# Kernel tuning notes

Measured on AMD Instinct MI355X. Metric: run time of the kernel, lower is better.

## Reference

```python
import jax, jax.numpy as jnp
import numpy as np
from jax import lax

INPUT_DIM = 12
T = 2048
H = 512
L = 6
EPS = 1e-5


def setup_inputs() -> dict:
    key = jax.random.key(0)
    ks = jax.random.split(key, 12)
    s = 1.0 / np.sqrt(H)
    inp = {
        "x": jax.random.normal(ks[0], (32, INPUT_DIM), dtype=jnp.float32),
        "in_proj_w": jax.random.normal(ks[1], (H, INPUT_DIM), dtype=jnp.float32) * (1.0 / np.sqrt(INPUT_DIM)),
        "in_proj_b": jnp.zeros((H,), dtype=jnp.float32),
        "W_ih": jax.random.uniform(ks[2], (L, 4 * H, H), dtype=jnp.float32, minval=-s, maxval=s),
        "W_hh": jax.random.uniform(ks[3], (L, 4 * H, H), dtype=jnp.float32, minval=-s, maxval=s),
        "b_ih": jax.random.uniform(ks[4], (L, 4 * H), dtype=jnp.float32, minval=-s, maxval=s),
        "b_hh": jax.random.uniform(ks[5], (L, 4 * H), dtype=jnp.float32, minval=-s, maxval=s),
        "ln_scale": jnp.ones((L, H), dtype=jnp.float32),
        "ln_bias": jnp.zeros((L, H), dtype=jnp.float32),
        "out_w": jax.random.normal(ks[6], (1, H), dtype=jnp.float32) * s,
        "out_b": jnp.zeros((1,), dtype=jnp.float32),
    }
    return inp


def _lstm_layer(h_in, Wih, Whh, bih, bhh):
    # h_in: (B, T, H); PyTorch gate order: i, f, g, o
    B = h_in.shape[0]
    xg = jnp.einsum("bth,gh->btg", h_in, Wih) + bih  # (B, T, 4H) input gates precomputed
    xg_t = jnp.swapaxes(xg, 0, 1)  # (T, B, 4H)
    h0 = jnp.zeros((B, H), dtype=h_in.dtype)
    c0 = jnp.zeros((B, H), dtype=h_in.dtype)

    def step(carry, xt):
        h, c = carry
        gates = xt + h @ Whh.T + bhh
        i, f, g, o = jnp.split(gates, 4, axis=-1)
        i = jax.nn.sigmoid(i)
        f = jax.nn.sigmoid(f)
        g = jnp.tanh(g)
        o = jax.nn.sigmoid(o)
        c = f * c + i * g
        h = o * jnp.tanh(c)
        return (h, c), h

    _, hs = lax.scan(step, (h0, c0), xg_t)  # hs: (T, B, H)
    return jnp.swapaxes(hs, 0, 1)


def _layernorm(x, scale, bias):
    mu = jnp.mean(x, axis=-1, keepdims=True)
    var = jnp.mean(jnp.square(x - mu), axis=-1, keepdims=True)
    return (x - mu) * lax.rsqrt(var + EPS) * scale + bias


def reference(x, in_proj_w, in_proj_b, W_ih, W_hh, b_ih, b_hh, ln_scale, ln_bias, out_w, out_b):
    x_proj = x @ in_proj_w.T + in_proj_b  # (B, H)
    h = jnp.broadcast_to(x_proj[:, None, :], (x.shape[0], T, H))  # repeat along time
    for l in range(L):
        out = _lstm_layer(h, W_ih[l], W_hh[l], b_ih[l], b_hh[l])
        h = _layernorm(out + h, ln_scale[l], ln_bias[l])  # dropout = identity (eval)
    y = jnp.einsum("bth,oh->bto", h, out_w) + out_b  # (B, T, 1)
    return y[..., 0]  # (B, T)
```

## Files before the change

kernel.cpp:

```cpp
#include <hip/hip_runtime.h>

typedef __attribute__((ext_vector_type(4))) int   i32x4;
typedef __attribute__((ext_vector_type(8))) short s16x8;
typedef __attribute__((ext_vector_type(4))) float f32x4;

__device__ __forceinline__ unsigned short f2bf(float f) {
  unsigned u = __float_as_uint(f);
  unsigned r = u + 0x7FFFu + ((u >> 16) & 1u);
  return (unsigned short)(r >> 16);
}
__device__ __forceinline__ unsigned pack2bf(float lo, float hi) {
  return (unsigned)f2bf(lo) | ((unsigned)f2bf(hi) << 16);
}
__device__ __forceinline__ float bflo(unsigned u){ return __uint_as_float(u << 16); }
__device__ __forceinline__ float bfhi(unsigned u){ return __uint_as_float(u & 0xFFFF0000u); }

__device__ __forceinline__ float sigm(float x){ return 1.0f / (1.0f + __expf(-x)); }
__device__ __forceinline__ float tanh_(float x){
  float ax = fabsf(x);
  float e  = __expf(-2.0f * ax);
  float t  = (1.0f - e) / (1.0f + e);
  return copysignf(t, x);
}

__device__ __forceinline__ unsigned long long aload(const unsigned long long* p) {
  return __hip_atomic_load(p, __ATOMIC_RELAXED, __HIP_MEMORY_SCOPE_AGENT);
}
__device__ __forceinline__ void astore32(unsigned* p, unsigned v) {
  __hip_atomic_store(p, v, __ATOMIC_RELAXED, __HIP_MEMORY_SCOPE_AGENT);
}
__device__ __forceinline__ void astore64(unsigned long long* p, unsigned long long v) {
  __hip_atomic_store(p, v, __ATOMIC_RELAXED, __HIP_MEMORY_SCOPE_AGENT);
}

__device__ __forceinline__ void waitflags(const unsigned* Flg, int base, unsigned need, int lane) {
  const unsigned* p = Flg + ((base + (lane & 31)) << 4);
  unsigned v = __hip_atomic_load(p, __ATOMIC_RELAXED, __HIP_MEMORY_SCOPE_AGENT);
  while (!__all((int)(v >= need))) {
    __builtin_amdgcn_s_sleep(1);
    v = __hip_atomic_load(p, __ATOMIC_RELAXED, __HIP_MEMORY_SCOPE_AGENT);
  }
}

__global__ __launch_bounds__(256) void k_inproj(const float* __restrict__ x,
                                                const float* __restrict__ w,
                                                const float* __restrict__ bb,
                                                float* __restrict__ XP) {
  int idx = blockIdx.x * 256 + threadIdx.x;
  int b = idx >> 9, j = idx & 511;
  float acc = bb[j];
#pragma unroll
  for (int k = 0; k < 12; ++k) acc += x[b * 12 + k] * w[j * 12 + k];
  XP[idx] = acc;
}

__global__ __launch_bounds__(256) void k_xg0(const float* __restrict__ XP,
                                             const float* __restrict__ Wih,
                                             const float* __restrict__ bih,
                                             float* __restrict__ XG0) {
  int idx = blockIdx.x * 256 + threadIdx.x;
  int b = idx & 31;
  int r = idx >> 5;
  const float* wr = Wih + (size_t)r * 512;
  const float* xr = XP + b * 512;
  float acc = bih[r];
  for (int k = 0; k < 512; k += 4) {
    const f32x4 w4 = *(const f32x4*)(wr + k);
    const f32x4 x4 = *(const f32x4*)(xr + k);
    acc += w4[0]*x4[0] + w4[1]*x4[1] + w4[2]*x4[2] + w4[3]*x4[3];
  }
  XG0[b * 2048 + r] = acc;
}

__global__ __launch_bounds__(256, 1) void k_pipe(
    const float* __restrict__ Wih, const float* __restrict__ Whh,
    const float* __restrict__ bih, const float* __restrict__ bhh,
    const float* __restrict__ lnS, const float* __restrict__ lnB,
    const float* __restrict__ XG0, const float* __restrict__ XP,
    unsigned long long* __restrict__ Hst,
    unsigned long long* __restrict__ Roll,
    unsigned long long* __restrict__ Part,
    unsigned* __restrict__ RB,
    unsigned* __restrict__ Flg,
    unsigned* __restrict__ Prog)
{
  __shared__ char smem[65536];
  const int tid   = threadIdx.x;
  const int wgid  = blockIdx.x;
  const int layer = wgid >> 5;
  const int w     = wgid & 31;

  char* xarea = smem;
  char* harea = smem + 32768;
  const int lane = tid & 63;
  const int wv   = tid >> 6;
  const int j0   = w << 4;
  float* gacc = (float*)(layer == 0 ? (smem + 10240) : (harea + 16384));

  unsigned long long* HstL = Hst + layer * 8192;

  s16x8 bfih[16], bfhh[16];
  {
    const int rcol = lane & 15;
    const int kg   = lane >> 4;
    const size_t rowbase = ((size_t)layer * 2048 + (size_t)(wv * 512 + j0 + rcol)) * 512;
    const float* ihr = Wih + rowbase;
    const float* hhr = Whh + rowbase;
#pragma unroll
    for (int kk = 0; kk < 16; ++kk) {
      const int k0 = kg * 8 + kk * 32;
      s16x8 v2;
#pragma unroll
      for (int j = 0; j < 8; ++j) v2[j] = (short)f2bf(hhr[k0 + j]);
      bfhh[kk] = v2;
      if (layer > 0) {
        s16x8 v1;
#pragma unroll
        for (int j = 0; j < 8; ++j) v1[j] = (short)f2bf(ihr[k0 + j]);
        bfih[kk] = v1;
      }
    }
  }

  const int ub = tid >> 3;
  const int jp = tid & 7;
  const int kpglob = (j0 >> 1) + jp;

  float bs[4][2];
#pragma unroll
  for (int g = 0; g < 4; ++g)
#pragma unroll
    for (int c = 0; c < 2; ++c) {
      const size_t r = (size_t)layer * 2048 + g * 512 + j0 + 2 * jp + c;
      float vv = bhh[r];
      if (layer > 0) vv += bih[r];
      bs[g][c] = vv;
    }

  float scp[4] = {0,0,0,0}, bip[4] = {0,0,0,0};
  if (layer > 0) {
    const int cb = (layer - 1) * 512 + 4 * (tid & 127);
#pragma unroll
    for (int j = 0; j < 4; ++j) { scp[j] = lnS[cb + j]; bip[j] = lnB[cb + j]; }
  }

  if (layer == 0) {
    float* xg0s = (float*)smem;
    float* xps  = (float*)(smem + 8192);
    for (int i = tid; i < 2048; i += 256) {
      int g = i >> 9, b = (i >> 4) & 31, jl = i & 15;
      xg0s[i] = XG0[b * 2048 + g * 512 + j0 + jl];
    }
    for (int i = tid; i < 512; i += 256) {
      int b = i >> 4, jl = i & 15;
      xps[i] = XP[b * 512 + j0 + jl];
    }
  }

  astore32((unsigned*)HstL + (ub << 8) + kpglob, 0u);
  __syncthreads();
  if (tid == 0)
    __hip_atomic_store(Flg + ((layer * 32 + w) << 4), 1u, __ATOMIC_RELEASE, __HIP_MEMORY_SCOPE_AGENT);

  float xinc0 = 0.f, xinc1 = 0.f;
  if (layer == 0) {
    const float* xps = (const float*)(smem + 8192);
    xinc0 = xps[ub * 16 + 2 * jp];
    xinc1 = xps[ub * 16 + 2 * jp + 1];
  }

  const int b31 = tid & 31, w8 = tid >> 5;

  if (layer > 0) {
    waitflags(Flg, (layer - 1) * 32, 2u, lane);
    const unsigned long long* RollC = Roll + (layer - 1) * 16384;
    const unsigned long long* PC    = Part + (layer - 1) * 4096;
    unsigned long long xr[16], pr[4];
#pragma unroll
    for (int it = 0; it < 16; ++it) xr[it] = aload(RollC + it * 256 + tid);
#pragma unroll
    for (int k = 0; k < 4; ++k) pr[k] = aload(PC + (w8 + 8 * k) * 32 + b31);
    float s4 = 0.f, ss4 = 0.f;
#pragma unroll
    for (int k = 0; k < 4; ++k) { s4 += __uint_as_float((unsigned)pr[k]); ss4 += __uint_as_float((unsigned)(pr[k] >> 32)); }
    float* scr = (float*)harea;
    scr[(w8 * 32 + b31) * 2]     = s4;
    scr[(w8 * 32 + b31) * 2 + 1] = ss4;
    __syncthreads();
    float* stats = (float*)(harea + 2048);
    if (tid < 32) {
      const float* sc = (const float*)harea;
      float ssum = 0.f, sssum = 0.f;
#pragma unroll
      for (int k = 0; k < 8; ++k) { ssum += sc[(k * 32 + tid) * 2]; sssum += sc[(k * 32 + tid) * 2 + 1]; }
      const float mu = ssum * (1.f / 512.f);
      float var = sssum * (1.f / 512.f) - mu * mu;
      stats[tid * 2] = mu; stats[tid * 2 + 1] = rsqrtf(var + 1e-5f);
    }
    __syncthreads();
#pragma unroll
    for (int it = 0; it < 16; ++it) {
      const int flat = it * 256 + tid;
      const int q = flat >> 7, c0 = (flat & 127) * 2;
      const float mu = stats[q * 2], rs = stats[q * 2 + 1];
      const unsigned lo = (unsigned)xr[it], hi = (unsigned)(xr[it] >> 32);
      const float a0 = (bflo(lo) - mu) * rs * scp[0] + bip[0];
      const float a1 = (bfhi(lo) - mu) * rs * scp[1] + bip[1];
      const float a2 = (bflo(hi) - mu) * rs * scp[2] + bip[2];
      const float a3 = (bfhi(hi) - mu) * rs * scp[3] + bip[3];
      *(unsigned long long*)(xarea + ((q * 1024 + c0 * 4) ^ ((q & 7) << 4))) =
          (unsigned long long)pack2bf(a0, a1) | ((unsigned long long)pack2bf(a2, a3) << 32);
    }
  }
  __syncthreads();

  const int rA  = lane & 15;
  const int kg2 = lane >> 4;
  const int swz = (rA & 7) << 4;
  const int ab0 = rA * 1024 + kg2 * 16;
  const int ab1 = ab0 + 16384;

  float creg0 = 0.f, creg1 = 0.f;
  unsigned myC = 0;
  const int lane31 = lane & 31;

#pragma unroll 1
  for (int t = 0; t < 2048; ++t) {
    if (layer < 5 && t >= 5) {
      const unsigned need = (unsigned)(t - 4);
      while (!__all((int)(myC >= need))) {
        if (myC < need)
          myC = __hip_atomic_load(Prog + (((layer + 1) * 32 + lane31) << 4),
                                  __ATOMIC_RELAXED, __HIP_MEMORY_SCOPE_AGENT);
        if (!__all((int)(myC >= need))) __builtin_amdgcn_s_sleep(1);
      }
    }

    waitflags(Flg, layer * 32, (unsigned)(t + 1), lane);

    const unsigned long long* hs = HstL + (size_t)(t & 1) * 4096;
    unsigned long long a[16];
#pragma unroll
    for (int it = 0; it < 16; ++it)
      a[it] = aload(hs + it * 256 + tid);

    float xin0, xin1;
    f32x4 ai0 = {0.f,0.f,0.f,0.f}, ai1 = {0.f,0.f,0.f,0.f};
    if (layer > 0) {
      const unsigned xu = *(const unsigned*)(xarea + (((ub * 1024) + kpglob * 4) ^ ((ub & 7) << 4)));
      xin0 = bflo(xu); xin1 = bfhi(xu);
#pragma unroll
      for (int kk = 0; kk < 16; ++kk) {
        const i32x4 x0 = *(const i32x4*)(xarea + ((ab0 + kk * 64) ^ swz));
        const i32x4 x1 = *(const i32x4*)(xarea + ((ab1 + kk * 64) ^ swz));
        ai0 = __builtin_amdgcn_mfma_f32_16x16x32_bf16(__builtin_bit_cast(s16x8, x0), bfih[kk], ai0, 0, 0, 0);
        ai1 = __builtin_amdgcn_mfma_f32_16x16x32_bf16(__builtin_bit_cast(s16x8, x1), bfih[kk], ai1, 0, 0, 0);
      }
    } else { xin0 = xinc0; xin1 = xinc1; }

#pragma unroll
    for (int it = 0; it < 16; ++it) {
      const int flat = it * 256 + tid;
      const int q = flat >> 7, kp2 = flat & 127;
      *(unsigned long long*)(harea + ((q * 1024 + kp2 * 8) ^ ((q & 7) << 4))) = a[it];
    }
    __syncthreads();

    f32x4 acc0, acc1;
    if (layer > 0) {
      f32x4 ah0 = {0.f,0.f,0.f,0.f}, ah1 = {0.f,0.f,0.f,0.f};
#pragma unroll
      for (int kk = 0; kk < 16; ++kk) {
        const i32x4 h0 = *(const i32x4*)(harea + ((ab0 + kk * 64) ^ swz));
        const i32x4 h1 = *(const i32x4*)(harea + ((ab1 + kk * 64) ^ swz));
        ah0 = __builtin_amdgcn_mfma_f32_16x16x32_bf16(__builtin_bit_cast(s16x8, h0), bfhh[kk], ah0, 0, 0, 0);
        ah1 = __builtin_amdgcn_mfma_f32_16x16x32_bf16(__builtin_bit_cast(s16x8, h1), bfhh[kk], ah1, 0, 0, 0);
      }
      acc0 = ai0 + ah0; acc1 = ai1 + ah1;
    } else {
      f32x4 a0a = {0.f,0.f,0.f,0.f}, a1a = {0.f,0.f,0.f,0.f};
      f32x4 a0b = {0.f,0.f,0.f,0.f}, a1b = {0.f,0.f,0.f,0.f};
#pragma unroll
      for (int kk = 0; kk < 8; ++kk) {
        const i32x4 h0a = *(const i32x4*)(harea + ((ab0 + kk * 64) ^ swz));
        const i32x4 h1a = *(const i32x4*)(harea + ((ab1 + kk * 64) ^ swz));
        const i32x4 h0b = *(const i32x4*)(harea + ((ab0 + (kk + 8) * 64) ^ swz));
        const i32x4 h1b = *(const i32x4*)(harea + ((ab1 + (kk + 8) * 64) ^ swz));
        a0a = __builtin_amdgcn_mfma_f32_16x16x32_bf16(__builtin_bit_cast(s16x8, h0a), bfhh[kk], a0a, 0, 0, 0);
        a1a = __builtin_amdgcn_mfma_f32_16x16x32_bf16(__builtin_bit_cast(s16x8, h1a), bfhh[kk], a1a, 0, 0, 0);
        a0b = __builtin_amdgcn_mfma_f32_16x16x32_bf16(__builtin_bit_cast(s16x8, h0b), bfhh[kk + 8], a0b, 0, 0, 0);
        a1b = __builtin_amdgcn_mfma_f32_16x16x32_bf16(__builtin_bit_cast(s16x8, h1b), bfhh[kk + 8], a1b, 0, 0, 0);
      }
      acc0 = a0a + a0b; acc1 = a1a + a1b;
    }
    __syncthreads();
    {
      float* gp = gacc + (wv * 16 + rA) * 36 + kg2 * 4;
      *(f32x4*)gp        = acc0;
      *(f32x4*)(gp + 16) = acc1;
    }
    __syncthreads();

    float pre[4][2];
#pragma unroll
    for (int g = 0; g < 4; ++g)
#pragma unroll
      for (int c = 0; c < 2; ++c) {
        float vv = gacc[(g * 16 + 2 * jp + c) * 36 + ub] + bs[g][c];
        if (layer == 0) vv += ((const float*)smem)[(g * 32 + ub) * 16 + 2 * jp + c];
        pre[g][c] = vv;
      }

    float i0 = sigm(pre[0][0]), ff0 = sigm(pre[1][0]), g0 = tanh_(pre[2][0]), o0 = sigm(pre[3][0]);
    creg0 = ff0 * creg0 + i0 * g0;
    float h0 = o0 * tanh_(creg0);
    float i1 = sigm(pre[0][1]), ff1 = sigm(pre[1][1]), g1 = tanh_(pre[2][1]), o1 = sigm(pre[3][1]);
    creg1 = ff1 * creg1 + i1 * g1;
    float h1 = o1 * tanh_(creg1);
    const float out0 = h0 + xin0, out1 = h1 + xin1;

    if (layer < 5) {
      float sP  = out0 + out1;
      float ssP = out0 * out0 + out1 * out1;
#pragma unroll
      for (int m = 1; m < 8; m <<= 1) { sP += __shfl_xor(sP, m, 64); ssP += __shfl_xor(ssP, m, 64); }
      astore32((unsigned*)(Roll + layer * 16384 + (size_t)(t & 3) * 4096) + (ub << 8) + kpglob,
               pack2bf(out0, out1));
      if (jp == 0)
        astore64(Part + layer * 4096 + (size_t)(t & 3) * 1024 + w * 32 + ub,
                 (unsigned long long)__float_as_uint(sP) |
                 ((unsigned long long)__float_as_uint(ssP) << 32));
    } else {
      RB[((size_t)ub * 2048 + t) * 256 + kpglob] = pack2bf(out0, out1);
    }
    astore32((unsigned*)(HstL + (size_t)((t + 1) & 1) * 4096) + (ub << 8) + kpglob,
             pack2bf(h0, h1));

    __syncthreads();
    if (tid == 0)
      __hip_atomic_store(Flg + ((layer * 32 + w) << 4), (unsigned)(t + 2),
                         __ATOMIC_RELEASE, __HIP_MEMORY_SCOPE_AGENT);

    if (layer > 0 && t < 2047) {
      waitflags(Flg, (layer - 1) * 32, (unsigned)(t + 3), lane);
      const unsigned long long* RollC = Roll + (layer - 1) * 16384 + (size_t)((t + 1) & 3) * 4096;
      const unsigned long long* PC    = Part + (layer - 1) * 4096 + (size_t)((t + 1) & 3) * 1024;
      unsigned long long xr[16], pr[4];
#pragma unroll
      for (int it = 0; it < 16; ++it) xr[it] = aload(RollC + it * 256 + tid);
#pragma unroll
      for (int k = 0; k < 4; ++k) pr[k] = aload(PC + (w8 + 8 * k) * 32 + b31);
      float s4 = 0.f, ss4 = 0.f;
#pragma unroll
      for (int k = 0; k < 4; ++k) { s4 += __uint_as_float((unsigned)pr[k]); ss4 += __uint_as_float((unsigned)(pr[k] >> 32)); }
      float* scr = (float*)harea;
      scr[(w8 * 32 + b31) * 2]     = s4;
      scr[(w8 * 32 + b31) * 2 + 1] = ss4;
      __syncthreads();
      float* stats = (float*)(harea + 2048);
      if (tid < 32) {
        const float* sc = (const float*)harea;
        float ssum = 0.f, sssum = 0.f;
#pragma unroll
        for (int k = 0; k < 8; ++k) { ssum += sc[(k * 32 + tid) * 2]; sssum += sc[(k * 32 + tid) * 2 + 1]; }
        const float mu = ssum * (1.f / 512.f);
        float var = sssum * (1.f / 512.f) - mu * mu;
        stats[tid * 2] = mu; stats[tid * 2 + 1] = rsqrtf(var + 1e-5f);
      }
      __syncthreads();
#pragma unroll
      for (int it = 0; it < 16; ++it) {
        const int flat = it * 256 + tid;
        const int q = flat >> 7, c0 = (flat & 127) * 2;
        const float mu = stats[q * 2], rs = stats[q * 2 + 1];
        const unsigned lo = (unsigned)xr[it], hi = (unsigned)(xr[it] >> 32);
        const float a0 = (bflo(lo) - mu) * rs * scp[0] + bip[0];
        const float a1 = (bfhi(lo) - mu) * rs * scp[1] + bip[1];
        const float a2 = (bflo(hi) - mu) * rs * scp[2] + bip[2];
        const float a3 = (bfhi(hi) - mu) * rs * scp[3] + bip[3];
        *(unsigned long long*)(xarea + ((q * 1024 + c0 * 4) ^ ((q & 7) << 4))) =
            (unsigned long long)pack2bf(a0, a1) | ((unsigned long long)pack2bf(a2, a3) << 32);
      }
      if (tid == 0)
        astore32(Prog + ((layer * 32 + w) << 4), (unsigned)(t + 1));
    }

    __syncthreads();
  }
}

__global__ __launch_bounds__(256) void k_lnout(const unsigned* __restrict__ Rin,
                                               const float* __restrict__ lnS,
                                               const float* __restrict__ lnB,
                                               const float* __restrict__ ow,
                                               const float* __restrict__ ob,
                                               float* __restrict__ y) {
  int row  = blockIdx.x * 4 + (threadIdx.x >> 6);
  int lane = threadIdx.x & 63;
  const i32x4 v = *(const i32x4*)(Rin + (size_t)row * 256 + lane * 4);
  float xv[8];
#pragma unroll
  for (int j = 0; j < 4; ++j) {
    unsigned u = (unsigned)v[j];
    xv[2*j]   = bflo(u);
    xv[2*j+1] = bfhi(u);
  }
  float s = 0.f, s2 = 0.f;
#pragma unroll
  for (int j = 0; j < 8; ++j) { s += xv[j]; s2 += xv[j] * xv[j]; }
#pragma unroll
  for (int m = 1; m < 64; m <<= 1) { s += __shfl_xor(s, m, 64); s2 += __shfl_xor(s2, m, 64); }
  float mu  = s * (1.f / 512.f);
  float var = s2 * (1.f / 512.f) - mu * mu;
  float rs  = rsqrtf(var + 1e-5f);
  const float* Sp = lnS + 5 * 512 + lane * 8;
  const float* Bp = lnB + 5 * 512 + lane * 8;
  const float* wp = ow + lane * 8;
  float acc = 0.f;
#pragma unroll
  for (int j = 0; j < 8; ++j)
    acc += ((xv[j] - mu) * rs * Sp[j] + Bp[j]) * wp[j];
#pragma unroll
  for (int m = 1; m < 64; m <<= 1) acc += __shfl_xor(acc, m, 64);
  if (lane == 0) y[row] = acc + ob[0];
}

extern "C" void kernel_launch(void* const* d_in, const int* in_sizes, int n_in,
                              void* d_out, int out_size, void* d_ws, size_t ws_size,
                              hipStream_t stream) {
  (void)in_sizes; (void)n_in; (void)out_size; (void)ws_size;
  const float* x   = (const float*)d_in[0];
  const float* ipw = (const float*)d_in[1];
  const float* ipb = (const float*)d_in[2];
  const float* Wih = (const float*)d_in[3];
  const float* Whh = (const float*)d_in[4];
  const float* bih = (const float*)d_in[5];
  const float* bhh = (const float*)d_in[6];
  const float* lnS = (const float*)d_in[7];
  const float* lnB = (const float*)d_in[8];
  const float* ow  = (const float*)d_in[9];
  const float* ob  = (const float*)d_in[10];
  float* y = (float*)d_out;

  char* ws = (char*)d_ws;
  unsigned* Flg             = (unsigned*)ws;
  unsigned* Prog            = (unsigned*)(ws + 16384);
  float* XP                 = (float*)(ws + 32768);
  float* XG0                = (float*)(ws + 98304);
  unsigned long long* Hst   = (unsigned long long*)(ws + 360448);
  unsigned long long* Roll  = (unsigned long long*)(ws + 753664);
  unsigned long long* Part  = (unsigned long long*)(ws + 1409024);
  unsigned* RB              = (unsigned*)(ws + 2097152);

  hipMemsetAsync(ws, 0, 32768, stream);
  k_inproj<<<64, 256, 0, stream>>>(x, ipw, ipb, XP);
  k_xg0<<<256, 256, 0, stream>>>(XP, Wih, bih, XG0);
  k_pipe<<<192, 256, 0, stream>>>(Wih, Whh, bih, bhh, lnS, lnB, XG0, XP,
                                  Hst, Roll, Part, RB, Flg, Prog);
  k_lnout<<<16384, 256, 0, stream>>>(RB, lnS, lnB, ow, ob, y);
}
```

Before: 18.25 ms.

## Compute layernorm stats locally per consumer, drop partial-sum exchange and barriers

Producers no longer publish per-block partial sums and sums of squares for the inter-layer layernorm. Each consumer loads a full 512-wide row per group of 8 lanes and reduces the statistics itself with wave shuffles, which removes the Part buffer, two __syncthreads and an LDS scratch reduction from every timestep. The wait and load of the next timestep's input is also moved ahead of the barrier and flag release, so it overlaps with the end of the current step. In exchange, the layernorm scale and bias are now read from global memory every step, and variance is computed from bf16-rounded values.

```diff
diff --git a/kernel.cpp b/kernel.cpp
--- a/kernel.cpp
+++ b/kernel.cpp
@@ -29,12 +29,9 @@
 __device__ __forceinline__ void astore32(unsigned* p, unsigned v) {
   __hip_atomic_store(p, v, __ATOMIC_RELAXED, __HIP_MEMORY_SCOPE_AGENT);
 }
-__device__ __forceinline__ void astore64(unsigned long long* p, unsigned long long v) {
-  __hip_atomic_store(p, v, __ATOMIC_RELAXED, __HIP_MEMORY_SCOPE_AGENT);
-}
-
-__device__ __forceinline__ void waitflags(const unsigned* Flg, int base, unsigned need, int lane) {
-  const unsigned* p = Flg + ((base + (lane & 31)) << 4);
+
+__device__ __forceinline__ void waitflags(const unsigned* F, int base, unsigned need, int lane) {
+  const unsigned* p = F + ((base + (lane & 31)) << 4);
   unsigned v = __hip_atomic_load(p, __ATOMIC_RELAXED, __HIP_MEMORY_SCOPE_AGENT);
   while (!__all((int)(v >= need))) {
     __builtin_amdgcn_s_sleep(1);
@@ -79,7 +76,6 @@
     const float* __restrict__ XG0, const float* __restrict__ XP,
     unsigned long long* __restrict__ Hst,
     unsigned long long* __restrict__ Roll,
-    unsigned long long* __restrict__ Part,
     unsigned* __restrict__ RB,
     unsigned* __restrict__ Flg,
     unsigned* __restrict__ Prog)
@@ -137,12 +133,8 @@
       bs[g][c] = vv;
     }
 
-  float scp[4] = {0,0,0,0}, bip[4] = {0,0,0,0};
-  if (layer > 0) {
-    const int cb = (layer - 1) * 512 + 4 * (tid & 127);
-#pragma unroll
-    for (int j = 0; j < 4; ++j) { scp[j] = lnS[cb + j]; bip[j] = lnB[cb + j]; }
-  }
+  const float* lnSl = lnS + (layer - 1) * 512;
+  const float* lnBl = lnB + (layer - 1) * 512;
 
   if (layer == 0) {
     float* xg0s = (float*)smem;
@@ -169,46 +161,38 @@
     xinc1 = xps[ub * 16 + 2 * jp + 1];
   }
 
-  const int b31 = tid & 31, w8 = tid >> 5;
+  const int rr  = tid >> 3;
+  const int kk8 = tid & 7;
 
   if (layer > 0) {
     waitflags(Flg, (layer - 1) * 32, 2u, lane);
     const unsigned long long* RollC = Roll + (layer - 1) * 16384;
-    const unsigned long long* PC    = Part + (layer - 1) * 4096;
-    unsigned long long xr[16], pr[4];
-#pragma unroll
-    for (int it = 0; it < 16; ++it) xr[it] = aload(RollC + it * 256 + tid);
-#pragma unroll
-    for (int k = 0; k < 4; ++k) pr[k] = aload(PC + (w8 + 8 * k) * 32 + b31);
-    float s4 = 0.f, ss4 = 0.f;
-#pragma unroll
-    for (int k = 0; k < 4; ++k) { s4 += __uint_as_float((unsigned)pr[k]); ss4 += __uint_as_float((unsigned)(pr[k] >> 32)); }
-    float* scr = (float*)harea;
-    scr[(w8 * 32 + b31) * 2]     = s4;
-    scr[(w8 * 32 + b31) * 2 + 1] = ss4;
-    __syncthreads();
-    float* stats = (float*)(harea + 2048);
-    if (tid < 32) {
-      const float* sc = (const float*)harea;
-      float ssum = 0.f, sssum = 0.f;
-#pragma unroll
-      for (int k = 0; k < 8; ++k) { ssum += sc[(k * 32 + tid) * 2]; sssum += sc[(k * 32 + tid) * 2 + 1]; }
-      const float mu = ssum * (1.f / 512.f);
-      float var = sssum * (1.f / 512.f) - mu * mu;
-      stats[tid * 2] = mu; stats[tid * 2 + 1] = rsqrtf(var + 1e-5f);
-    }
-    __syncthreads();
-#pragma unroll
-    for (int it = 0; it < 16; ++it) {
-      const int flat = it * 256 + tid;
-      const int q = flat >> 7, c0 = (flat & 127) * 2;
-      const float mu = stats[q * 2], rs = stats[q * 2 + 1];
-      const unsigned lo = (unsigned)xr[it], hi = (unsigned)(xr[it] >> 32);
-      const float a0 = (bflo(lo) - mu) * rs * scp[0] + bip[0];
-      const float a1 = (bfhi(lo) - mu) * rs * scp[1] + bip[1];
-      const float a2 = (bflo(hi) - mu) * rs * scp[2] + bip[2];
-      const float a3 = (bfhi(hi) - mu) * rs * scp[3] + bip[3];
-      *(unsigned long long*)(xarea + ((q * 1024 + c0 * 4) ^ ((q & 7) << 4))) =
+    unsigned long long xr[16];
+#pragma unroll
+    for (int j = 0; j < 16; ++j) xr[j] = aload(RollC + rr * 128 + kk8 + 8 * j);
+    float s = 0.f, ss = 0.f;
+#pragma unroll
+    for (int j = 0; j < 16; ++j) {
+      const unsigned lo = (unsigned)xr[j], hi = (unsigned)(xr[j] >> 32);
+      const float v0 = bflo(lo), v1 = bfhi(lo), v2 = bflo(hi), v3 = bfhi(hi);
+      s  += v0 + v1 + v2 + v3;
+      ss += v0 * v0 + v1 * v1 + v2 * v2 + v3 * v3;
+    }
+#pragma unroll
+    for (int m = 1; m < 8; m <<= 1) { s += __shfl_xor(s, m, 64); ss += __shfl_xor(ss, m, 64); }
+    const float mu = s * (1.f / 512.f);
+    const float rs = rsqrtf(ss * (1.f / 512.f) - mu * mu + 1e-5f);
+#pragma unroll
+    for (int j = 0; j < 16; ++j) {
+      const int jj = kk8 + 8 * j;
+      const f32x4 sc4 = *(const f32x4*)(lnSl + 4 * jj);
+      const f32x4 bi4 = *(const f32x4*)(lnBl + 4 * jj);
+      const unsigned lo = (unsigned)xr[j], hi = (unsigned)(xr[j] >> 32);
+      const float a0 = (bflo(lo) - mu) * rs * sc4[0] + bi4[0];
+      const float a1 = (bfhi(lo) - mu) * rs * sc4[1] + bi4[1];
+      const float a2 = (bflo(hi) - mu) * rs * sc4[2] + bi4[2];
+      const float a3 = (bfhi(hi) - mu) * rs * sc4[3] + bi4[3];
+      *(unsigned long long*)(xarea + ((rr * 1024 + jj * 8) ^ ((rr & 7) << 4))) =
           (unsigned long long)pack2bf(a0, a1) | ((unsigned long long)pack2bf(a2, a3) << 32);
     }
   }
@@ -320,69 +304,56 @@
     const float out0 = h0 + xin0, out1 = h1 + xin1;
 
     if (layer < 5) {
-      float sP  = out0 + out1;
-      float ssP = out0 * out0 + out1 * out1;
-#pragma unroll
-      for (int m = 1; m < 8; m <<= 1) { sP += __shfl_xor(sP, m, 64); ssP += __shfl_xor(ssP, m, 64); }
-      astore32((unsigned*)(Roll + layer * 16384 + (size_t)(t & 3) * 4096) + (ub << 8) + kpglob,
+      astore32((unsigned*)(Roll + (size_t)(layer * 4 + (t & 3)) * 4096) + (ub << 8) + kpglob,
                pack2bf(out0, out1));
-      if (jp == 0)
-        astore64(Part + layer * 4096 + (size_t)(t & 3) * 1024 + w * 32 + ub,
-                 (unsigned long long)__float_as_uint(sP) |
-                 ((unsigned long long)__float_as_uint(ssP) << 32));
     } else {
       RB[((size_t)ub * 2048 + t) * 256 + kpglob] = pack2bf(out0, out1);
     }
     astore32((unsigned*)(HstL + (size_t)((t + 1) & 1) * 4096) + (ub << 8) + kpglob,
              pack2bf(h0, h1));
 
+    unsigned long long xr[16];
+    if (layer > 0 && t < 2047) {
+      waitflags(Flg, (layer - 1) * 32, (unsigned)(t + 3), lane);
+      const unsigned long long* RollC = Roll + (size_t)((layer - 1) * 4 + ((t + 1) & 3)) * 4096;
+#pragma unroll
+      for (int j = 0; j < 16; ++j) xr[j] = aload(RollC + rr * 128 + kk8 + 8 * j);
+    }
+
     __syncthreads();
-    if (tid == 0)
+    if (tid == 0) {
       __hip_atomic_store(Flg + ((layer * 32 + w) << 4), (unsigned)(t + 2),
                          __ATOMIC_RELEASE, __HIP_MEMORY_SCOPE_AGENT);
+      if (layer > 0 && t < 2047)
+        astore32(Prog + ((layer * 32 + w) << 4), (unsigned)(t + 1));
+    }
 
     if (layer > 0 && t < 2047) {
-      waitflags(Flg, (layer - 1) * 32, (unsigned)(t + 3), lane);
-      const unsigned long long* RollC = Roll + (layer - 1) * 16384 + (size_t)((t + 1) & 3) * 4096;
-      const unsigned long long* PC    = Part + (layer - 1) * 4096 + (size_t)((t + 1) & 3) * 1024;
-      unsigned long long xr[16], pr[4];
-#pragma unroll
-      for (int it = 0; it < 16; ++it) xr[it] = aload(RollC + it * 256 + tid);
-#pragma unroll
-      for (int k = 0; k < 4; ++k) pr[k] = aload(PC + (w8 + 8 * k) * 32 + b31);
-      float s4 = 0.f, ss4 = 0.f;
-#pragma unroll
-      for (int k = 0; k < 4; ++k) { s4 += __uint_as_float((unsigned)pr[k]); ss4 += __uint_as_float((unsigned)(pr[k] >> 32)); }
-      float* scr = (float*)harea;
-      scr[(w8 * 32 + b31) * 2]     = s4;
-      scr[(w8 * 32 + b31) * 2 + 1] = ss4;
-      __syncthreads();
-      float* stats = (float*)(harea + 2048);
-      if (tid < 32) {
-        const float* sc = (const float*)harea;
-        float ssum = 0.f, sssum = 0.f;
-#pragma unroll
-        for (int k = 0; k < 8; ++k) { ssum += sc[(k * 32 + tid) * 2]; sssum += sc[(k * 32 + tid) * 2 + 1]; }
-        const float mu = ssum * (1.f / 512.f);
-        float var = sssum * (1.f / 512.f) - mu * mu;
-        stats[tid * 2] = mu; stats[tid * 2 + 1] = rsqrtf(var + 1e-5f);
-      }
-      __syncthreads();
-#pragma unroll
-      for (int it = 0; it < 16; ++it) {
-        const int flat = it * 256 + tid;
-        const int q = flat >> 7, c0 = (flat & 127) * 2;
-        const float mu = stats[q * 2], rs = stats[q * 2 + 1];
-        const unsigned lo = (unsigned)xr[it], hi = (unsigned)(xr[it] >> 32);
-        const float a0 = (bflo(lo) - mu) * rs * scp[0] + bip[0];
-        const float a1 = (bfhi(lo) - mu) * rs * scp[1] + bip[1];
-        const float a2 = (bflo(hi) - mu) * rs * scp[2] + bip[2];
-        const float a3 = (bfhi(hi) - mu) * rs * scp[3] + bip[3];
-        *(unsigned long long*)(xarea + ((q * 1024 + c0 * 4) ^ ((q & 7) << 4))) =
+      float s = 0.f, ss = 0.f;
+#pragma unroll
+      for (int j = 0; j < 16; ++j) {
+        const unsigned lo = (unsigned)xr[j], hi = (unsigned)(xr[j] >> 32);
+        const float v0 = bflo(lo), v1 = bfhi(lo), v2 = bflo(hi), v3 = bfhi(hi);
+        s  += v0 + v1 + v2 + v3;
+        ss += v0 * v0 + v1 * v1 + v2 * v2 + v3 * v3;
+      }
+#pragma unroll
+      for (int m = 1; m < 8; m <<= 1) { s += __shfl_xor(s, m, 64); ss += __shfl_xor(ss, m, 64); }
+      const float mu = s * (1.f / 512.f);
+      const float rs = rsqrtf(ss * (1.f / 512.f) - mu * mu + 1e-5f);
+#pragma unroll
+      for (int j = 0; j < 16; ++j) {
+        const int jj = kk8 + 8 * j;
+        const f32x4 sc4 = *(const f32x4*)(lnSl + 4 * jj);
+        const f32x4 bi4 = *(const f32x4*)(lnBl + 4 * jj);
+        const unsigned lo = (unsigned)xr[j], hi = (unsigned)(xr[j] >> 32);
+        const float a0 = (bflo(lo) - mu) * rs * sc4[0] + bi4[0];
+        const float a1 = (bfhi(lo) - mu) * rs * sc4[1] + bi4[1];
+        const float a2 = (bflo(hi) - mu) * rs * sc4[2] + bi4[2];
+        const float a3 = (bfhi(hi) - mu) * rs * sc4[3] + bi4[3];
+        *(unsigned long long*)(xarea + ((rr * 1024 + jj * 8) ^ ((rr & 7) << 4))) =
             (unsigned long long)pack2bf(a0, a1) | ((unsigned long long)pack2bf(a2, a3) << 32);
       }
-      if (tid == 0)
-        astore32(Prog + ((layer * 32 + w) << 4), (unsigned)(t + 1));
     }
 
     __syncthreads();
@@ -449,13 +420,12 @@
   float* XG0                = (float*)(ws + 98304);
   unsigned long long* Hst   = (unsigned long long*)(ws + 360448);
   unsigned long long* Roll  = (unsigned long long*)(ws + 753664);
-  unsigned long long* Part  = (unsigned long long*)(ws + 1409024);
   unsigned* RB              = (unsigned*)(ws + 2097152);
 
   hipMemsetAsync(ws, 0, 32768, stream);
   k_inproj<<<64, 256, 0, stream>>>(x, ipw, ipb, XP);
   k_xg0<<<256, 256, 0, stream>>>(XP, Wih, bih, XG0);
   k_pipe<<<192, 256, 0, stream>>>(Wih, Whh, bih, bhh, lnS, lnB, XG0, XP,
-                                  Hst, Roll, Part, RB, Flg, Prog);
+                                  Hst, Roll, RB, Flg, Prog);
   k_lnout<<<16384, 256, 0, stream>>>(RB, lnS, lnB, ow, ob, y);
 }
```

Measured after the change: 17.37 ms. 1.05x faster.
